# Kernel optimization log

Hardware: AMD Instinct MI355X
Metric: run time of the kernel (lower is better)

Reference implementation:

```python
import jax, jax.numpy as jnp
import numpy as np

EMBED_DIM = 768
NUM_HEADS = 12
HEAD_DIM = EMBED_DIM // NUM_HEADS
MEMORY_SIZE = 64
B, T = 8, 1024


def setup_inputs() -> dict:
    key = jax.random.key(0)
    ks = jax.random.split(key, 8)
    s = 0.02
    return {
        "x": jax.random.normal(ks[0], (B, T, EMBED_DIM), dtype=jnp.float32),
        "w_qkv": jax.random.normal(ks[1], (EMBED_DIM, 3 * EMBED_DIM), dtype=jnp.float32) * s,
        "b_qkv": jax.random.normal(ks[2], (3 * EMBED_DIM,), dtype=jnp.float32) * s,
        "w_out": jax.random.normal(ks[3], (EMBED_DIM, EMBED_DIM), dtype=jnp.float32) * s,
        "b_out": jax.random.normal(ks[4], (EMBED_DIM,), dtype=jnp.float32) * s,
        "w_mem": jax.random.normal(ks[5], (EMBED_DIM, EMBED_DIM), dtype=jnp.float32) * s,
        "b_mem": jax.random.normal(ks[6], (EMBED_DIM,), dtype=jnp.float32) * s,
        "memory": jax.random.normal(ks[7], (1, MEMORY_SIZE, EMBED_DIM), dtype=jnp.float32),
    }


def reference(x, w_qkv, b_qkv, w_out, b_out, w_mem, b_mem, memory):
    Bx, Tx, C = x.shape
    H, D = NUM_HEADS, HEAD_DIM
    scale = 1.0 / np.sqrt(D).astype(np.float32)

    # qkv projection -> (3, B, H, T, D)
    qkv = (x @ w_qkv + b_qkv).reshape(Bx, Tx, 3, H, D)
    qkv = jnp.transpose(qkv, (2, 0, 3, 1, 4))
    q, k, v = qkv[0], qkv[1], qkv[2]

    # full (non-causal) local attention over T
    scores = jnp.einsum("bhqd,bhkd->bhqk", q, k) * scale  # (B,H,T,T)
    local_out = jnp.einsum("bhqk,bhkd->bhqd", jax.nn.softmax(scores, axis=-1), v)

    # memory attention: projected memory serves as both K and V
    mem = memory @ w_mem + b_mem                      # (1, M, C)
    mem = jnp.broadcast_to(mem, (Bx, MEMORY_SIZE, C))
    mem_kv = jnp.transpose(mem.reshape(Bx, MEMORY_SIZE, H, D), (0, 2, 1, 3))  # (B,H,M,D)
    mem_scores = jnp.einsum("bhqd,bhmd->bhqm", q, mem_kv) * scale
    mem_out = jnp.einsum("bhqm,bhmd->bhqd", jax.nn.softmax(mem_scores, axis=-1), mem_kv)

    out = (local_out + mem_out).transpose(0, 2, 1, 3).reshape(Bx, Tx, C)
    return out @ w_out + b_out
```

## Files before the change

kernel.cpp:

```cpp
#include <hip/hip_runtime.h>

#define EMBED 768
#define NH 12
#define HD 64
#define MEMN 64
#define BB 8
#define TT 1024
#define ROWS 8192
#define QKV_N 2304
#define QSZ 6291456

typedef short bf16x8_t __attribute__((ext_vector_type(8)));
typedef float f32x4_t __attribute__((ext_vector_type(4)));

__device__ __forceinline__ unsigned short f2b(float f){
    union { float f; unsigned int i; } v; v.f = f;
    unsigned int x = v.i;
    unsigned int r = x + 0x7fffu + ((x >> 16) & 1u);
    return (unsigned short)(r >> 16);
}
__device__ __forceinline__ unsigned short f2b_ru(float f){
    union { float f; unsigned int i; } v; v.f = f;
    return (unsigned short)((v.i + 0x8000u) >> 16);
}

__device__ __forceinline__ void gl16(const unsigned short* g, unsigned short* l){
    __builtin_amdgcn_global_load_lds(
        (const __attribute__((address_space(1))) void*)g,
        (__attribute__((address_space(3))) void*)l,
        16, 0, 0);
}

#define SCHED_FENCE() __builtin_amdgcn_sched_barrier(0)

#define PREP_CVT   3072
#define PREP_TQKV  4800
#define PREP_TOUT  5376
#define PREP_TOTAL 5388

__global__ __launch_bounds__(256) void prep_kernel(
    const float* __restrict__ x,
    const float* __restrict__ w_qkv,
    const float* __restrict__ w_out,
    const float* __restrict__ memory,
    const float* __restrict__ w_mem,
    const float* __restrict__ b_mem,
    unsigned short* __restrict__ xb,
    unsigned short* __restrict__ wqkvT,
    unsigned short* __restrict__ woutT,
    unsigned short* __restrict__ mem_k,
    unsigned short* __restrict__ mem_v)
{
    __shared__ unsigned short pool[5120];
    const int bid = blockIdx.x;
    const int t = threadIdx.x;

    if (bid < PREP_CVT) {
        int i = bid * 2048 + t * 8;
        float4 f0 = *(const float4*)&x[i];
        float4 f1 = *(const float4*)&x[i + 4];
        union { bf16x8_t v; unsigned short s[8]; } u;
        u.s[0] = f2b(f0.x); u.s[1] = f2b(f0.y); u.s[2] = f2b(f0.z); u.s[3] = f2b(f0.w);
        u.s[4] = f2b(f1.x); u.s[5] = f2b(f1.y); u.s[6] = f2b(f1.z); u.s[7] = f2b(f1.w);
        *(bf16x8_t*)&xb[i] = u.v;
    } else if (bid < PREP_TOUT) {
        const float* in; unsigned short* out; int R, C, loc;
        if (bid < PREP_TQKV) { in = w_qkv; out = wqkvT; R = EMBED; C = QKV_N; loc = bid - PREP_CVT; }
        else                 { in = w_out; out = woutT; R = EMBED; C = EMBED; loc = bid - PREP_TQKV; }
        int nbc = C / 32;
        int bc = (loc % nbc) * 32, br = (loc / nbc) * 32;
        unsigned short (*tile)[33] = (unsigned short(*)[33])pool;
        int lr = t >> 5, lc = t & 31;
        for (int i = 0; i < 4; i++) {
            int r = lr + i * 8;
            tile[r][lc] = f2b(in[(size_t)(br + r) * C + bc + lc]);
        }
        __syncthreads();
        for (int i = 0; i < 4; i++) {
            int r = lr + i * 8;
            out[(size_t)(bc + r) * R + br + lc] = tile[lc][r];
        }
    } else {
        unsigned short (*As)[40] = (unsigned short(*)[40])pool;
        unsigned short (*Bs)[40] = (unsigned short(*)[40])(pool + 2560);
        int wave = t >> 6, lane = t & 63;
        int ln = lane & 15, lq = lane >> 4;
        int bn = (bid - PREP_TOUT) * 64;
        const int K = EMBED, N = EMBED;

        f32x4_t acc[4];
        for (int i = 0; i < 4; i++) acc[i] = (f32x4_t)(0.f);
        int sm = t >> 2, sk = (t & 3) * 8;
        int bk = t >> 3, bn8 = (t & 7) * 8;

        for (int k0 = 0; k0 < K; k0 += 32) {
            __syncthreads();
            {
                float4 f0 = *(const float4*)&memory[(size_t)sm * K + k0 + sk];
                float4 f1 = *(const float4*)&memory[(size_t)sm * K + k0 + sk + 4];
                unsigned short* ap = &As[sm][sk];
                ap[0] = f2b(f0.x); ap[1] = f2b(f0.y); ap[2] = f2b(f0.z); ap[3] = f2b(f0.w);
                ap[4] = f2b(f1.x); ap[5] = f2b(f1.y); ap[6] = f2b(f1.z); ap[7] = f2b(f1.w);
            }
            {
                float4 g0 = *(const float4*)&w_mem[(size_t)(k0 + bk) * N + bn + bn8];
                float4 g1 = *(const float4*)&w_mem[(size_t)(k0 + bk) * N + bn + bn8 + 4];
                Bs[bn8 + 0][bk] = f2b(g0.x); Bs[bn8 + 1][bk] = f2b(g0.y);
                Bs[bn8 + 2][bk] = f2b(g0.z); Bs[bn8 + 3][bk] = f2b(g0.w);
                Bs[bn8 + 4][bk] = f2b(g1.x); Bs[bn8 + 5][bk] = f2b(g1.y);
                Bs[bn8 + 6][bk] = f2b(g1.z); Bs[bn8 + 7][bk] = f2b(g1.w);
            }
            __syncthreads();
            bf16x8_t a = *(bf16x8_t*)&As[wave * 16 + ln][lq * 8];
            for (int nt = 0; nt < 4; nt++) {
                bf16x8_t bf = *(bf16x8_t*)&Bs[nt * 16 + ln][lq * 8];
                acc[nt] = __builtin_amdgcn_mfma_f32_16x16x32_bf16(a, bf, acc[nt], 0, 0, 0);
            }
        }
        for (int nt = 0; nt < 4; nt++) {
            int c = bn + nt * 16 + ln;
            float bv = b_mem[c];
            for (int r = 0; r < 4; r++) {
                int row = wave * 16 + lq * 4 + r;
                int h = c >> 6, d = c & 63;
                unsigned short o = f2b(acc[nt][r] + bv);
                mem_k[((h * 64 + row) << 6) + d] = o;
                mem_v[((h * 64 + d) << 6) + row] = o;
            }
        }
    }
}

__global__ __launch_bounds__(256) void vtrans_kernel(
    const unsigned short* __restrict__ in, unsigned short* __restrict__ out)
{
    __shared__ unsigned short tile[64][72];
    int t0 = blockIdx.x * 64;
    int bh = blockIdx.y;
    const unsigned short* ip = in + ((size_t)bh * TT + t0) * 64;
    unsigned short* op = out + ((size_t)bh * 64) * TT + t0;
    int t = threadIdx.x;
    for (int i = 0; i < 2; i++) {
        int idx = i * 256 + t;
        int r = idx >> 3, c8 = (idx & 7) * 8;
        *(bf16x8_t*)&tile[r][c8] = *(const bf16x8_t*)&ip[(size_t)r * 64 + c8];
    }
    __syncthreads();
    for (int i = 0; i < 2; i++) {
        int idx = i * 256 + t;
        int d = idx >> 3, tc8 = (idx & 7) * 8;
        union { bf16x8_t v; unsigned short s[8]; } u;
        for (int j = 0; j < 8; j++) u.s[j] = tile[tc8 + j][d];
        *(bf16x8_t*)&op[(size_t)d * TT + tc8] = u.v;
    }
}

__global__ __launch_bounds__(512) void gemm512(
    const unsigned short* __restrict__ A,
    const unsigned short* __restrict__ BT,
    const float* __restrict__ bias,
    unsigned short* __restrict__ dq,
    unsigned short* __restrict__ dkv,
    int M, int N, int K)
{
    __shared__ unsigned short As[2][16384];
    __shared__ unsigned short Bs[2][8192];
    const int t = threadIdx.x;
    const int wave = t >> 6, lane = t & 63;
    const int ln = lane & 15, lq = lane >> 4;
    const int wm = (wave >> 1) * 64, wn = (wave & 1) * 64;

    int bid0 = blockIdx.y * gridDim.x + blockIdx.x;
    int bid = (bid0 & 7) * 72 + (bid0 >> 3);
    int by = bid / 18, bx = bid - by * 18;
    const int bm = by * 256, bn = bx * 128;

    f32x4_t acc[4][4];
    for (int i = 0; i < 4; i++)
        for (int j = 0; j < 4; j++) acc[i][j] = (f32x4_t)(0.f);

    const int rl8 = lane >> 3;
    const int swz = ((lane & 7) ^ rl8) * 8;
    const unsigned short* Ap = A + (size_t)(bm + wave * 32 + rl8) * 768 + swz;
    const unsigned short* Bp = BT + (size_t)(bn + wave * 16 + rl8) * 768 + swz;

    const int e0 = (lq ^ (ln & 7)) * 8;
    const int e1 = e0 ^ 32;

    auto stage = [&](int buf, int k0) {
#pragma unroll
        for (int i = 0; i < 4; i++)
            gl16(Ap + (size_t)(i * 8) * 768 + k0, &As[buf][wave * 2048 + i * 512]);
#pragma unroll
        for (int i = 0; i < 2; i++)
            gl16(Bp + (size_t)(i * 8) * 768 + k0, &Bs[buf][wave * 1024 + i * 512]);
    };

    auto compute = [&](const unsigned short* Ac, const unsigned short* Bc) {
        bf16x8_t af0[4], af1[4], bf0[4], bf1[4];
#pragma unroll
        for (int mt = 0; mt < 4; mt++) {
            af0[mt] = *(const bf16x8_t*)&Ac[(wm + mt * 16 + ln) * 64 + e0];
            af1[mt] = *(const bf16x8_t*)&Ac[(wm + mt * 16 + ln) * 64 + e1];
        }
#pragma unroll
        for (int nt = 0; nt < 4; nt++) {
            bf0[nt] = *(const bf16x8_t*)&Bc[(wn + nt * 16 + ln) * 64 + e0];
            bf1[nt] = *(const bf16x8_t*)&Bc[(wn + nt * 16 + ln) * 64 + e1];
        }
        __builtin_amdgcn_s_setprio(1);
#pragma unroll
        for (int mt = 0; mt < 4; mt++)
#pragma unroll
            for (int nt = 0; nt < 4; nt++)
                acc[mt][nt] = __builtin_amdgcn_mfma_f32_16x16x32_bf16(
                    af0[mt], bf0[nt], acc[mt][nt], 0, 0, 0);
#pragma unroll
        for (int mt = 0; mt < 4; mt++)
#pragma unroll
            for (int nt = 0; nt < 4; nt++)
                acc[mt][nt] = __builtin_amdgcn_mfma_f32_16x16x32_bf16(
                    af1[mt], bf1[nt], acc[mt][nt], 0, 0, 0);
        __builtin_amdgcn_s_setprio(0);
    };

    stage(0, 0);
    stage(1, 64);
    SCHED_FENCE();
    asm volatile("s_waitcnt vmcnt(6)" ::: "memory");
    SCHED_FENCE();
    __builtin_amdgcn_s_barrier();
    SCHED_FENCE();

#pragma unroll 2
    for (int tt = 0; tt < 10; ++tt) {
        const int cur = tt & 1;
        compute(&As[cur][0], &Bs[cur][0]);
        SCHED_FENCE();
        __builtin_amdgcn_s_barrier();
        SCHED_FENCE();
        stage(cur, (tt + 2) * 64);
        SCHED_FENCE();
        asm volatile("s_waitcnt vmcnt(6)" ::: "memory");
        SCHED_FENCE();
        __builtin_amdgcn_s_barrier();
        SCHED_FENCE();
    }
    compute(&As[0][0], &Bs[0][0]);
    SCHED_FENCE();
    asm volatile("s_waitcnt vmcnt(0)" ::: "memory");
    SCHED_FENCE();
    __builtin_amdgcn_s_barrier();
    SCHED_FENCE();
    compute(&As[1][0], &Bs[1][0]);

    const float QSCALE = 0.125f * 1.44269504088896340736f;
    const int s = bn / 768;
    for (int nt = 0; nt < 4; nt++) {
        int c = bn + wn + nt * 16 + ln;
        int rem = c - s * 768;
        int h = rem >> 6, d = rem & 63;
        float bv = bias[c];
        for (int mt = 0; mt < 4; mt++) {
            for (int r = 0; r < 4; r++) {
                int row = bm + wm + mt * 16 + lq * 4 + r;
                float val = acc[mt][nt][r] + bv;
                if (s == 0) {
                    dq[(size_t)row * 768 + rem] = f2b(val * QSCALE);
                } else {
                    int bb = row >> 10, tt2 = row & 1023;
                    dkv[(size_t)(s - 1) * QSZ +
                        (((size_t)(bb * 12 + h) * 1024 + tt2) << 6) + d] = f2b(val);
                }
            }
        }
    }
}

__global__ __launch_bounds__(256) void gemm_bt(
    const unsigned short* __restrict__ A,
    const unsigned short* __restrict__ BT,
    const float* __restrict__ bias,
    float* __restrict__ df,
    int M, int N, int K)
{
    __shared__ unsigned short As[2][8192];
    __shared__ unsigned short Bs[2][8192];
    const int t = threadIdx.x;
    const int wave = t >> 6, lane = t & 63;
    const int ln = lane & 15, lq = lane >> 4;
    const int wm = (wave >> 1) * 64, wn = (wave & 1) * 64;
    const int bm = blockIdx.y * 128, bn = blockIdx.x * 128;

    f32x4_t acc[4][4];
    for (int i = 0; i < 4; i++)
        for (int j = 0; j < 4; j++) acc[i][j] = (f32x4_t)(0.f);

    const int rl8 = lane >> 3;
    const int swz = ((lane & 7) ^ rl8) * 8;
    const unsigned short* Ap = A + (size_t)(bm + wave * 32 + rl8) * 768 + swz;
    const unsigned short* Bp = BT + (size_t)(bn + wave * 32 + rl8) * 768 + swz;

    const int e0 = (lq ^ (ln & 7)) * 8;
    const int e1 = e0 ^ 32;

    auto stage = [&](int buf, int k0) {
#pragma unroll
        for (int i = 0; i < 4; i++) {
            gl16(Ap + (size_t)(i * 8) * 768 + k0, &As[buf][wave * 2048 + i * 512]);
            gl16(Bp + (size_t)(i * 8) * 768 + k0, &Bs[buf][wave * 2048 + i * 512]);
        }
    };

    auto compute = [&](const unsigned short* Ac, const unsigned short* Bc) {
        bf16x8_t af0[4], af1[4], bf0[4], bf1[4];
#pragma unroll
        for (int mt = 0; mt < 4; mt++) {
            af0[mt] = *(const bf16x8_t*)&Ac[(wm + mt * 16 + ln) * 64 + e0];
            af1[mt] = *(const bf16x8_t*)&Ac[(wm + mt * 16 + ln) * 64 + e1];
        }
#pragma unroll
        for (int nt = 0; nt < 4; nt++) {
            bf0[nt] = *(const bf16x8_t*)&Bc[(wn + nt * 16 + ln) * 64 + e0];
            bf1[nt] = *(const bf16x8_t*)&Bc[(wn + nt * 16 + ln) * 64 + e1];
        }
        __builtin_amdgcn_s_setprio(1);
#pragma unroll
        for (int mt = 0; mt < 4; mt++)
#pragma unroll
            for (int nt = 0; nt < 4; nt++)
                acc[mt][nt] = __builtin_amdgcn_mfma_f32_16x16x32_bf16(
                    af0[mt], bf0[nt], acc[mt][nt], 0, 0, 0);
#pragma unroll
        for (int mt = 0; mt < 4; mt++)
#pragma unroll
            for (int nt = 0; nt < 4; nt++)
                acc[mt][nt] = __builtin_amdgcn_mfma_f32_16x16x32_bf16(
                    af1[mt], bf1[nt], acc[mt][nt], 0, 0, 0);
        __builtin_amdgcn_s_setprio(0);
    };

    stage(0, 0);
    stage(1, 64);
    SCHED_FENCE();
    asm volatile("s_waitcnt vmcnt(8)" ::: "memory");
    SCHED_FENCE();
    __builtin_amdgcn_s_barrier();
    SCHED_FENCE();

#pragma unroll 2
    for (int tt = 0; tt < 10; ++tt) {
        const int cur = tt & 1;
        compute(&As[cur][0], &Bs[cur][0]);
        SCHED_FENCE();
        __builtin_amdgcn_s_barrier();
        SCHED_FENCE();
        stage(cur, (tt + 2) * 64);
        SCHED_FENCE();
        asm volatile("s_waitcnt vmcnt(8)" ::: "memory");
        SCHED_FENCE();
        __builtin_amdgcn_s_barrier();
        SCHED_FENCE();
    }
    compute(&As[0][0], &Bs[0][0]);
    SCHED_FENCE();
    asm volatile("s_waitcnt vmcnt(0)" ::: "memory");
    SCHED_FENCE();
    __builtin_amdgcn_s_barrier();
    SCHED_FENCE();
    compute(&As[1][0], &Bs[1][0]);

    for (int nt = 0; nt < 4; nt++) {
        int c = bn + wn + nt * 16 + ln;
        float bv = bias[c];
        for (int mt = 0; mt < 4; mt++)
            for (int r = 0; r < 4; r++) {
                int row = bm + wm + mt * 16 + lq * 4 + r;
                df[(size_t)row * N + c] = acc[mt][nt][r] + bv;
            }
    }
}

__global__ __launch_bounds__(512) void attn_kernel(
    unsigned short* __restrict__ qio,
    const unsigned short* __restrict__ k_ws,
    const unsigned short* __restrict__ vT_ws,
    const unsigned short* __restrict__ mem_k,
    const unsigned short* __restrict__ mem_v)
{
    __shared__ unsigned short Qs[8192];
    __shared__ unsigned short Ks[8192];
    __shared__ unsigned short Vs[8192];
    unsigned short* Ps = Qs;

    const int t = threadIdx.x;
    const int wave = t >> 6, lane = t & 63;
    const int ln = lane & 15, lq = lane >> 4;
    const int rl = lane >> 3;
    const int cl = ((lane & 7) ^ rl) * 8;

    int bid = blockIdx.x;
    int xcd = bid & 7, rest = bid >> 3;
    int bh = xcd * 12 + (rest >> 3);
    int qt = rest & 7;
    int b = bh / 12, h = bh - b * 12;

    unsigned short* qp = qio + ((size_t)(b * TT + qt * 128)) * 768 + h * 64;
    const unsigned short* kp = k_ws + (size_t)bh * TT * 64;
    const unsigned short* vp = vT_ws + ((size_t)bh << 16);
    const unsigned short* mkp = mem_k + h * 4096;
    const unsigned short* mvp = mem_v + h * 4096;

    {
        const unsigned short* qg = qp + (size_t)(wave * 16 + rl) * 768 + cl;
        gl16(qg, &Qs[wave * 1024]);
        gl16(qg + (size_t)8 * 768, &Qs[wave * 1024 + 512]);
    }
    __syncthreads();
    const int e0 = (lq ^ (ln & 7)) * 8;
    const int e1 = ((lq ^ (ln & 7)) ^ 4) * 8;
    bf16x8_t aq0 = *(bf16x8_t*)&Qs[(wave * 16 + ln) * 64 + e0];
    bf16x8_t aq1 = *(bf16x8_t*)&Qs[(wave * 16 + ln) * 64 + e1];

    const unsigned short* kg = kp + (wave * 16 + rl) * 64 + cl;
    const unsigned short* vg = vp + (size_t)((wave & 3) * 16 + rl) * 1024 + (wave >> 2) * 64 + cl;

    const int hi3 = ln >> 3, lo3 = ln & 7;
    const int pm = (lq & 1) << 2;
    const int pw0 = (wave * 16 + lq * 4) * 64 + lo3;

    float lsum[4] = {0.f, 0.f, 0.f, 0.f};
    f32x4_t accO[4];
    for (int nt = 0; nt < 4; nt++) accO[nt] = (f32x4_t)(0.f);

    for (int kt = 0; kt < 8; kt++) {
        __syncthreads();
        gl16(kg + kt * 8192,        &Ks[wave * 1024]);
        gl16(kg + kt * 8192 + 512,  &Ks[wave * 1024 + 512]);
        gl16(vg + kt * 128,                 &Vs[wave * 1024]);
        gl16(vg + (size_t)8 * 1024 + kt * 128, &Vs[wave * 1024 + 512]);
        __syncthreads();

        for (int half = 0; half < 2; half++) {
            const unsigned short* Kh = &Ks[half * 4096];
            const unsigned short* Vh = &Vs[half * 4096];
            f32x4_t s[4];
            for (int nt = 0; nt < 4; nt++) s[nt] = (f32x4_t)(0.f);
            for (int nt = 0; nt < 4; nt++)
                s[nt] = __builtin_amdgcn_mfma_f32_16x16x32_bf16(
                    aq0, *(bf16x8_t*)&Kh[(nt * 16 + ln) * 64 + e0], s[nt], 0, 0, 0);
            for (int nt = 0; nt < 4; nt++)
                s[nt] = __builtin_amdgcn_mfma_f32_16x16x32_bf16(
                    aq1, *(bf16x8_t*)&Kh[(nt * 16 + ln) * 64 + e1], s[nt], 0, 0, 0);

            for (int nt = 0; nt < 4; nt++) {
                for (int r = 0; r < 4; r++) {
                    float p = __builtin_amdgcn_exp2f(s[nt][r]);
                    lsum[r] += p;
                    int chp = (nt * 2 + hi3) ^ pm ^ r;
                    Ps[pw0 + r * 64 + chp * 8] = f2b_ru(p);
                }
            }
            bf16x8_t a0 = *(bf16x8_t*)&Ps[(wave * 16 + ln) * 64 + e0];
            bf16x8_t a1 = *(bf16x8_t*)&Ps[(wave * 16 + ln) * 64 + e1];
            for (int nt = 0; nt < 4; nt++) {
                accO[nt] = __builtin_amdgcn_mfma_f32_16x16x32_bf16(
                    a0, *(bf16x8_t*)&Vh[(nt * 16 + ln) * 64 + e0], accO[nt], 0, 0, 0);
                accO[nt] = __builtin_amdgcn_mfma_f32_16x16x32_bf16(
                    a1, *(bf16x8_t*)&Vh[(nt * 16 + ln) * 64 + e1], accO[nt], 0, 0, 0);
            }
        }
    }

    __syncthreads();
    gl16(mkp + (wave * 8 + rl) * 64 + cl, &Ks[wave * 512]);
    gl16(mvp + (wave * 8 + rl) * 64 + cl, &Vs[wave * 512]);
    __syncthreads();

    f32x4_t s2[4];
    for (int nt = 0; nt < 4; nt++) s2[nt] = (f32x4_t)(0.f);
    for (int nt = 0; nt < 4; nt++)
        s2[nt] = __builtin_amdgcn_mfma_f32_16x16x32_bf16(
            aq0, *(bf16x8_t*)&Ks[(nt * 16 + ln) * 64 + e0], s2[nt], 0, 0, 0);
    for (int nt = 0; nt < 4; nt++)
        s2[nt] = __builtin_amdgcn_mfma_f32_16x16x32_bf16(
            aq1, *(bf16x8_t*)&Ks[(nt * 16 + ln) * 64 + e1], s2[nt], 0, 0, 0);

    float l2[4] = {0.f, 0.f, 0.f, 0.f};
    for (int nt = 0; nt < 4; nt++) {
        for (int r = 0; r < 4; r++) {
            float p = __builtin_amdgcn_exp2f(s2[nt][r]);
            l2[r] += p;
            int chp = (nt * 2 + hi3) ^ pm ^ r;
            Ps[pw0 + r * 64 + chp * 8] = f2b_ru(p);
        }
    }
    f32x4_t accM[4];
    for (int nt = 0; nt < 4; nt++) accM[nt] = (f32x4_t)(0.f);
    {
        bf16x8_t a0 = *(bf16x8_t*)&Ps[(wave * 16 + ln) * 64 + e0];
        bf16x8_t a1 = *(bf16x8_t*)&Ps[(wave * 16 + ln) * 64 + e1];
        for (int nt = 0; nt < 4; nt++) {
            accM[nt] = __builtin_amdgcn_mfma_f32_16x16x32_bf16(
                a0, *(bf16x8_t*)&Vs[(nt * 16 + ln) * 64 + e0], accM[nt], 0, 0, 0);
            accM[nt] = __builtin_amdgcn_mfma_f32_16x16x32_bf16(
                a1, *(bf16x8_t*)&Vs[(nt * 16 + ln) * 64 + e1], accM[nt], 0, 0, 0);
        }
    }

    float inv[4], inv2[4];
    for (int r = 0; r < 4; r++) {
        float a = lsum[r], c = l2[r];
        a += __shfl_xor(a, 1); a += __shfl_xor(a, 2);
        a += __shfl_xor(a, 4); a += __shfl_xor(a, 8);
        c += __shfl_xor(c, 1); c += __shfl_xor(c, 2);
        c += __shfl_xor(c, 4); c += __shfl_xor(c, 8);
        inv[r] = 1.f / a;
        inv2[r] = 1.f / c;
    }

    for (int nt = 0; nt < 4; nt++) {
        for (int r = 0; r < 4; r++) {
            int lrow = wave * 16 + lq * 4 + r;
            int lcol = nt * 16 + ln;
            float val = accO[nt][r] * inv[r] + accM[nt][r] * inv2[r];
            qp[(size_t)lrow * 768 + lcol] = f2b(val);
        }
    }
}

extern "C" void kernel_launch(void* const* d_in, const int* in_sizes, int n_in,
                              void* d_out, int out_size, void* d_ws, size_t ws_size,
                              hipStream_t stream) {
    const float* x      = (const float*)d_in[0];
    const float* w_qkv  = (const float*)d_in[1];
    const float* b_qkv  = (const float*)d_in[2];
    const float* w_out  = (const float*)d_in[3];
    const float* b_out  = (const float*)d_in[4];
    const float* w_mem  = (const float*)d_in[5];
    const float* b_mem  = (const float*)d_in[6];
    const float* memory = (const float*)d_in[7];

    unsigned short* ws = (unsigned short*)d_ws;
    unsigned short* q_ws   = ws;
    unsigned short* k_ws   = ws + (size_t)QSZ;
    unsigned short* woutT  = ws + 3 * (size_t)QSZ;
    unsigned short* mem_k  = woutT + (size_t)EMBED * EMBED;
    unsigned short* mem_v  = mem_k + (size_t)NH * MEMN * HD;

    unsigned short* xb    = (unsigned short*)d_out;
    unsigned short* wqkvT = xb + (size_t)QSZ;
    unsigned short* vT    = (unsigned short*)d_out;

    prep_kernel<<<PREP_TOTAL, 256, 0, stream>>>(
        x, w_qkv, w_out, memory, w_mem, b_mem, xb, wqkvT, woutT, mem_k, mem_v);

    gemm512<<<dim3(QKV_N / 128, ROWS / 256), 512, 0, stream>>>(
        xb, wqkvT, b_qkv, q_ws, k_ws, ROWS, QKV_N, EMBED);

    vtrans_kernel<<<dim3(TT / 64, BB * NH), 256, 0, stream>>>(k_ws + (size_t)QSZ, vT);

    attn_kernel<<<8 * NH * BB, 512, 0, stream>>>(q_ws, k_ws, vT, mem_k, mem_v);

    gemm_bt<<<dim3(EMBED / 128, ROWS / 128), 256, 0, stream>>>(
        q_ws, woutT, b_out, (float*)d_out, ROWS, EMBED, EMBED);
}
```

Before: 246.5 us.

## Enlarge QKV GEMM tile to 256x256 with interleaved load/MFMA schedule

The QKV projection GEMM tile grows from 256x128 to 256x256, so each wave now computes a 128x64 sub-tile with 8x4 accumulators. The staging and compute loops are merged into a single fully unrolled 12-step K loop that issues next-tile global-to-LDS loads between MFMA groups to overlap memory traffic with math. This raises data reuse per LDS load and halves the grid to 288 blocks. In exchange it uses more registers and LDS, which can lower occupancy, and the smaller grid may underfill the 256 compute units.

```diff
diff --git a/kernel.cpp b/kernel.cpp
--- a/kernel.cpp
+++ b/kernel.cpp
@@ -164,104 +164,138 @@
     int M, int N, int K)
 {
     __shared__ unsigned short As[2][16384];
-    __shared__ unsigned short Bs[2][8192];
+    __shared__ unsigned short Bs[2][16384];
     const int t = threadIdx.x;
     const int wave = t >> 6, lane = t & 63;
     const int ln = lane & 15, lq = lane >> 4;
-    const int wm = (wave >> 1) * 64, wn = (wave & 1) * 64;
+    const int wm = (wave >> 2) * 128, wn = (wave & 3) * 64;
 
     int bid0 = blockIdx.y * gridDim.x + blockIdx.x;
-    int bid = (bid0 & 7) * 72 + (bid0 >> 3);
-    int by = bid / 18, bx = bid - by * 18;
-    const int bm = by * 256, bn = bx * 128;
-
-    f32x4_t acc[4][4];
-    for (int i = 0; i < 4; i++)
+    int bid = (bid0 & 7) * 36 + (bid0 >> 3);
+    int by = bid / 9, bx = bid - by * 9;
+    const int bm = by * 256, bn = bx * 256;
+
+    f32x4_t acc[8][4];
+#pragma unroll
+    for (int i = 0; i < 8; i++)
+#pragma unroll
         for (int j = 0; j < 4; j++) acc[i][j] = (f32x4_t)(0.f);
 
     const int rl8 = lane >> 3;
     const int swz = ((lane & 7) ^ rl8) * 8;
     const unsigned short* Ap = A + (size_t)(bm + wave * 32 + rl8) * 768 + swz;
-    const unsigned short* Bp = BT + (size_t)(bn + wave * 16 + rl8) * 768 + swz;
+    const unsigned short* Bp = BT + (size_t)(bn + wave * 32 + rl8) * 768 + swz;
 
     const int e0 = (lq ^ (ln & 7)) * 8;
     const int e1 = e0 ^ 32;
 
-    auto stage = [&](int buf, int k0) {
-#pragma unroll
-        for (int i = 0; i < 4; i++)
-            gl16(Ap + (size_t)(i * 8) * 768 + k0, &As[buf][wave * 2048 + i * 512]);
-#pragma unroll
-        for (int i = 0; i < 2; i++)
-            gl16(Bp + (size_t)(i * 8) * 768 + k0, &Bs[buf][wave * 1024 + i * 512]);
-    };
-
-    auto compute = [&](const unsigned short* Ac, const unsigned short* Bc) {
-        bf16x8_t af0[4], af1[4], bf0[4], bf1[4];
-#pragma unroll
-        for (int mt = 0; mt < 4; mt++) {
-            af0[mt] = *(const bf16x8_t*)&Ac[(wm + mt * 16 + ln) * 64 + e0];
-            af1[mt] = *(const bf16x8_t*)&Ac[(wm + mt * 16 + ln) * 64 + e1];
-        }
-#pragma unroll
-        for (int nt = 0; nt < 4; nt++) {
-            bf0[nt] = *(const bf16x8_t*)&Bc[(wn + nt * 16 + ln) * 64 + e0];
-            bf1[nt] = *(const bf16x8_t*)&Bc[(wn + nt * 16 + ln) * 64 + e1];
-        }
+#pragma unroll
+    for (int i = 0; i < 4; i++) {
+        gl16(Ap + (size_t)(i * 8) * 768, &As[0][wave * 2048 + i * 512]);
+        gl16(Bp + (size_t)(i * 8) * 768, &Bs[0][wave * 2048 + i * 512]);
+    }
+
+#pragma unroll
+    for (int kt2 = 0; kt2 < 12; ++kt2) {
+        const int buf = kt2 & 1, nbuf = buf ^ 1;
+        const int kn = (kt2 + 1) * 64;
+        const bool st = (kt2 < 11);
+
+        __builtin_amdgcn_s_barrier();
+        SCHED_FENCE();
+        if (st) {
+            gl16(Ap + kn,                        &As[nbuf][wave * 2048]);
+            gl16(Ap + (size_t)8 * 768 + kn,      &As[nbuf][wave * 2048 + 512]);
+        }
+        SCHED_FENCE();
+        if (st) asm volatile("s_waitcnt vmcnt(2)" ::: "memory");
+        else    asm volatile("s_waitcnt vmcnt(0)" ::: "memory");
+        SCHED_FENCE();
+        __builtin_amdgcn_s_barrier();
+        SCHED_FENCE();
+
+        bf16x8_t af[4], bf0[4], bf1[4];
+#pragma unroll
+        for (int j = 0; j < 4; j++) {
+            af[j]  = *(const bf16x8_t*)&As[buf][(wm + j * 16 + ln) * 64 + e0];
+            bf0[j] = *(const bf16x8_t*)&Bs[buf][(wn + j * 16 + ln) * 64 + e0];
+        }
+        if (st) {
+            gl16(Ap + (size_t)16 * 768 + kn,     &As[nbuf][wave * 2048 + 1024]);
+            gl16(Ap + (size_t)24 * 768 + kn,     &As[nbuf][wave * 2048 + 1536]);
+        }
+        SCHED_FENCE();
         __builtin_amdgcn_s_setprio(1);
 #pragma unroll
-        for (int mt = 0; mt < 4; mt++)
-#pragma unroll
-            for (int nt = 0; nt < 4; nt++)
-                acc[mt][nt] = __builtin_amdgcn_mfma_f32_16x16x32_bf16(
-                    af0[mt], bf0[nt], acc[mt][nt], 0, 0, 0);
-#pragma unroll
-        for (int mt = 0; mt < 4; mt++)
-#pragma unroll
-            for (int nt = 0; nt < 4; nt++)
-                acc[mt][nt] = __builtin_amdgcn_mfma_f32_16x16x32_bf16(
-                    af1[mt], bf1[nt], acc[mt][nt], 0, 0, 0);
+        for (int j = 0; j < 4; j++)
+#pragma unroll
+            for (int n2 = 0; n2 < 4; n2++)
+                acc[j][n2] = __builtin_amdgcn_mfma_f32_16x16x32_bf16(
+                    af[j], bf0[n2], acc[j][n2], 0, 0, 0);
         __builtin_amdgcn_s_setprio(0);
-    };
-
-    stage(0, 0);
-    stage(1, 64);
-    SCHED_FENCE();
-    asm volatile("s_waitcnt vmcnt(6)" ::: "memory");
-    SCHED_FENCE();
-    __builtin_amdgcn_s_barrier();
-    SCHED_FENCE();
-
-#pragma unroll 2
-    for (int tt = 0; tt < 10; ++tt) {
-        const int cur = tt & 1;
-        compute(&As[cur][0], &Bs[cur][0]);
-        SCHED_FENCE();
-        __builtin_amdgcn_s_barrier();
-        SCHED_FENCE();
-        stage(cur, (tt + 2) * 64);
-        SCHED_FENCE();
-        asm volatile("s_waitcnt vmcnt(6)" ::: "memory");
-        SCHED_FENCE();
-        __builtin_amdgcn_s_barrier();
-        SCHED_FENCE();
-    }
-    compute(&As[0][0], &Bs[0][0]);
-    SCHED_FENCE();
-    asm volatile("s_waitcnt vmcnt(0)" ::: "memory");
-    SCHED_FENCE();
-    __builtin_amdgcn_s_barrier();
-    SCHED_FENCE();
-    compute(&As[1][0], &Bs[1][0]);
+        SCHED_FENCE();
+#pragma unroll
+        for (int j = 0; j < 4; j++) {
+            af[j]  = *(const bf16x8_t*)&As[buf][(wm + j * 16 + ln) * 64 + e1];
+            bf1[j] = *(const bf16x8_t*)&Bs[buf][(wn + j * 16 + ln) * 64 + e1];
+        }
+        if (st) {
+            gl16(Bp + kn,                        &Bs[nbuf][wave * 2048]);
+            gl16(Bp + (size_t)8 * 768 + kn,      &Bs[nbuf][wave * 2048 + 512]);
+        }
+        SCHED_FENCE();
+        __builtin_amdgcn_s_setprio(1);
+#pragma unroll
+        for (int j = 0; j < 4; j++)
+#pragma unroll
+            for (int n2 = 0; n2 < 4; n2++)
+                acc[j][n2] = __builtin_amdgcn_mfma_f32_16x16x32_bf16(
+                    af[j], bf1[n2], acc[j][n2], 0, 0, 0);
+        __builtin_amdgcn_s_setprio(0);
+        SCHED_FENCE();
+#pragma unroll
+        for (int j = 0; j < 4; j++)
+            af[j] = *(const bf16x8_t*)&As[buf][(wm + (j + 4) * 16 + ln) * 64 + e0];
+        if (st) {
+            gl16(Bp + (size_t)16 * 768 + kn,     &Bs[nbuf][wave * 2048 + 1024]);
+            gl16(Bp + (size_t)24 * 768 + kn,     &Bs[nbuf][wave * 2048 + 1536]);
+        }
+        SCHED_FENCE();
+        __builtin_amdgcn_s_setprio(1);
+#pragma unroll
+        for (int j = 0; j < 4; j++)
+#pragma unroll
+            for (int n2 = 0; n2 < 4; n2++)
+                acc[j + 4][n2] = __builtin_amdgcn_mfma_f32_16x16x32_bf16(
+                    af[j], bf0[n2], acc[j + 4][n2], 0, 0, 0);
+        __builtin_amdgcn_s_setprio(0);
+        SCHED_FENCE();
+#pragma unroll
+        for (int j = 0; j < 4; j++)
+            af[j] = *(const bf16x8_t*)&As[buf][(wm + (j + 4) * 16 + ln) * 64 + e1];
+        SCHED_FENCE();
+        __builtin_amdgcn_s_setprio(1);
+#pragma unroll
+        for (int j = 0; j < 4; j++)
+#pragma unroll
+            for (int n2 = 0; n2 < 4; n2++)
+                acc[j + 4][n2] = __builtin_amdgcn_mfma_f32_16x16x32_bf16(
+                    af[j], bf1[n2], acc[j + 4][n2], 0, 0, 0);
+        __builtin_amdgcn_s_setprio(0);
+        SCHED_FENCE();
+    }
 
     const float QSCALE = 0.125f * 1.44269504088896340736f;
     const int s = bn / 768;
+#pragma unroll
     for (int nt = 0; nt < 4; nt++) {
         int c = bn + wn + nt * 16 + ln;
         int rem = c - s * 768;
         int h = rem >> 6, d = rem & 63;
         float bv = bias[c];
-        for (int mt = 0; mt < 4; mt++) {
+#pragma unroll
+        for (int mt = 0; mt < 8; mt++) {
+#pragma unroll
             for (int r = 0; r < 4; r++) {
                 int row = bm + wm + mt * 16 + lq * 4 + r;
                 float val = acc[mt][nt][r] + bv;
@@ -555,7 +589,7 @@
     prep_kernel<<<PREP_TOTAL, 256, 0, stream>>>(
         x, w_qkv, w_out, memory, w_mem, b_mem, xb, wqkvT, woutT, mem_k, mem_v);
 
-    gemm512<<<dim3(QKV_N / 128, ROWS / 256), 512, 0, stream>>>(
+    gemm512<<<dim3(QKV_N / 256, ROWS / 256), 512, 0, stream>>>(
         xb, wqkvT, b_qkv, q_ws, k_ws, ROWS, QKV_N, EMBED);
 
     vtrans_kernel<<<dim3(TT / 64, BB * NH), 256, 0, stream>>>(k_ws + (size_t)QSZ, vT);
```

New measurement: 250.6 us. No clear change (+1.6%).
